# Kernel tuning notes

Measured on AMD Instinct MI355X. Metric: run time of the kernel, lower is better.

Reference implementation:

```python
import jax, jax.numpy as jnp
import numpy as np

B, L, D = 2, 2048, 2048
NUM_HEADS, NUM_KV_HEADS, HEAD_DIM = 8, 4, 256
GROUPS = NUM_HEADS // NUM_KV_HEADS
ROPE_BASE, ROPE_SCALE, ROPE_PROP = 10000.0, 1.0, 1.0
WINDOW = 1024
SOFT_CAP = 50.0
K_MASK = -2.3819763e+38
EPS = 1e-6


def rms_norm(x, scale):
    # RMSNorm(head_dim, with_scale=True, scale_plus_one=False), fp32 internals
    xf = x.astype(jnp.float32)
    var = jnp.mean(jnp.square(xf), axis=-1, keepdims=True)
    return (xf * jax.lax.rsqrt(var + EPS) * scale).astype(x.dtype)


def apply_rope(x, positions):
    # x: [B, L, N, H]; Gemma-style half-split rotation over rope_proportion of H
    H = x.shape[-1]
    rope_dim = int(H * ROPE_PROP)
    half = rope_dim // 2
    freq = ROPE_BASE ** (2.0 * jnp.arange(half, dtype=jnp.float32) / rope_dim)
    t = positions.astype(jnp.float32)[:, :, None] / freq[None, None, :]  # [B,L,half]
    t = t / ROPE_SCALE
    sin = jnp.sin(t)[:, :, None, :]  # [B,L,1,half]
    cos = jnp.cos(t)[:, :, None, :]
    x1 = x[..., :half]
    x2 = x[..., half:rope_dim]
    rotated = jnp.concatenate([x1 * cos - x2 * sin, x2 * cos + x1 * sin], axis=-1)
    if rope_dim < H:
        rotated = jnp.concatenate([rotated, x[..., rope_dim:]], axis=-1)
    return rotated.astype(x.dtype)


def setup_inputs() -> dict:
    key = jax.random.key(0)
    ks = jax.random.split(key, 8)
    x = jax.random.normal(ks[0], (B, L, D), dtype=jnp.float32)
    positions = jnp.broadcast_to(jnp.arange(L, dtype=jnp.int32)[None, :], (B, L))
    attn_mask = jnp.broadcast_to(jnp.tril(jnp.ones((L, L), dtype=bool))[None], (B, L, L))
    s = 0.02
    wq = jax.random.normal(ks[1], (D, NUM_HEADS * HEAD_DIM), dtype=jnp.float32) * s
    wk = jax.random.normal(ks[2], (D, NUM_KV_HEADS * HEAD_DIM), dtype=jnp.float32) * s
    wv = jax.random.normal(ks[3], (D, NUM_KV_HEADS * HEAD_DIM), dtype=jnp.float32) * s
    wo = jax.random.normal(ks[4], (NUM_HEADS * HEAD_DIM, D), dtype=jnp.float32) * s
    q_scale = 1.0 + 0.02 * jax.random.normal(ks[5], (HEAD_DIM,), dtype=jnp.float32)
    k_scale = 1.0 + 0.02 * jax.random.normal(ks[6], (HEAD_DIM,), dtype=jnp.float32)
    return {"x": x, "positions": positions, "attn_mask": attn_mask,
            "wq": wq, "wk": wk, "wv": wv, "wo": wo,
            "q_scale": q_scale, "k_scale": k_scale}


def reference(x, positions, attn_mask, wq, wk, wv, wo, q_scale, k_scale):
    q = (x @ wq).reshape(B, L, NUM_HEADS, HEAD_DIM)
    k = (x @ wk).reshape(B, L, NUM_KV_HEADS, HEAD_DIM)
    v = (x @ wv).reshape(B, L, NUM_KV_HEADS, HEAD_DIM)
    q = rms_norm(q, q_scale)
    k = rms_norm(k, k_scale)
    q = apply_rope(q, positions)
    k = apply_rope(k, positions)
    # query_pre_attn_scalar == 1.0 in source (no-op)
    qg = q.reshape(B, L, NUM_KV_HEADS, GROUPS, HEAD_DIM)
    logits = jnp.einsum('blkgh,bskh->blkgs', qg, k).reshape(B, L, NUM_HEADS, L)
    logits = jnp.tanh(logits / SOFT_CAP) * SOFT_CAP
    # sliding-window mask (LOCAL_SLIDING, no cache -> cache_positions = positions)
    cp = positions[:, None, :]
    pp = positions[:, :, None]
    slide = (cp > pp - WINDOW) & (cp < pp + WINDOW)
    mask = attn_mask & slide  # [B, L, S]
    padded = jnp.where(mask[:, :, None, :], logits, K_MASK)
    probs = jax.nn.softmax(padded, axis=-1).astype(k.dtype)
    pg = probs.reshape(B, L, NUM_KV_HEADS, GROUPS, L)
    out = jnp.einsum('blkgs,bskh->blkgh', pg, v).reshape(B, L, NUM_HEADS * HEAD_DIM)
    return out @ wo
```

## Files before the change

kernel.cpp:

```cpp
#include <hip/hip_runtime.h>
#include <stdint.h>

typedef unsigned short u16;
typedef __bf16 bf16x8 __attribute__((ext_vector_type(8)));
typedef float f32x4 __attribute__((ext_vector_type(4)));

#define SEQ 2048
#define NH 8
#define NKVH 4
#define HD 256
#define WIN 1024
#define NBATCH 2

__device__ __forceinline__ u16 f2bf(float f) {
    union { float f; unsigned u; } v; v.f = f;
    unsigned r = v.u + 0x7FFFu + ((v.u >> 16) & 1u);
    return (u16)(r >> 16);
}
__device__ __forceinline__ float bf2f(u16 h) {
    union { unsigned u; float f; } v; v.u = ((unsigned)h) << 16;
    return v.f;
}
__device__ __forceinline__ bf16x8 ld8(const u16* p) {
    return *reinterpret_cast<const bf16x8*>(p);
}
__device__ __forceinline__ void split2(float f, u16& h, u16& l) {
    h = f2bf(f);
    l = f2bf(f - bf2f(h));
}
__device__ __forceinline__ void gld16(const u16* gp, u16* lp) {
    __builtin_amdgcn_global_load_lds(
        (__attribute__((address_space(1))) unsigned int*)gp,
        (__attribute__((address_space(3))) unsigned int*)lp, 16, 0, 0);
}
#define MFMA16(a, b, c) __builtin_amdgcn_mfma_f32_16x16x32_bf16((a), (b), (c), 0, 0, 0)

__global__ void k_cvt_x(const float* __restrict__ in, u16* __restrict__ hi,
                        u16* __restrict__ lo, int n) {
    int i = (blockIdx.x * blockDim.x + threadIdx.x) * 4;
    if (i >= n) return;
    float4 v = *reinterpret_cast<const float4*>(in + i);
    ushort4 oh, ol;
    split2(v.x, oh.x, ol.x); split2(v.y, oh.y, ol.y);
    split2(v.z, oh.z, ol.z); split2(v.w, oh.w, ol.w);
    *reinterpret_cast<ushort4*>(hi + i) = oh;
    *reinterpret_cast<ushort4*>(lo + i) = ol;
}

__global__ void k_wt(const float* __restrict__ src, u16* __restrict__ dh,
                     u16* __restrict__ dl, int ncols) {
    __shared__ float tile[64][65];
    int c0 = blockIdx.x * 64;
    int k0 = blockIdx.y * 64;
    int tx = threadIdx.x & 63, ty = threadIdx.x >> 6;
    #pragma unroll
    for (int r = 0; r < 16; ++r) {
        int k = k0 + ty * 16 + r;
        tile[ty * 16 + r][tx] = src[(size_t)k * ncols + c0 + tx];
    }
    __syncthreads();
    #pragma unroll
    for (int r = 0; r < 16; ++r) {
        int c = c0 + ty * 16 + r;
        float f = tile[tx][ty * 16 + r];
        u16 h, l; split2(f, h, l);
        dh[(size_t)c * 2048 + k0 + tx] = h;
        dl[(size_t)c * 2048 + k0 + tx] = l;
    }
}

__global__ __launch_bounds__(256, 4) void k_gemm(
        const u16* __restrict__ A0, const u16* __restrict__ B0,
        const u16* __restrict__ A1, const u16* __restrict__ B1,
        const u16* __restrict__ A2, const u16* __restrict__ B2,
        float* __restrict__ C, int M, int N, int K, int nseg, int vcol0) {
    __shared__ __align__(16) u16 sA[128 * 64];
    __shared__ __align__(16) u16 sB[128 * 64];
    const int tm = blockIdx.x * 128;
    const int tn = blockIdx.y * 128;
    const int tid = threadIdx.x;
    const int lane = tid & 63;
    const int wave = tid >> 6;
    const int wr = (wave >> 1) * 64;
    const int wc = (wave & 1) * 64;
    const int l16 = lane & 15;
    const int g = lane >> 4;
    const int srow = tid >> 3;
    const int schunk = tid & 7;
    const int nseg_eff = (tn >= vcol0) ? 1 : nseg;
    f32x4 acc[4][4] = {};

    for (int seg = 0; seg < nseg_eff; ++seg) {
        const u16* A = seg == 0 ? A0 : (seg == 1 ? A1 : A2);
        const u16* B = seg == 0 ? B0 : (seg == 1 ? B1 : B2);
        for (int k0 = 0; k0 < K; k0 += 64) {
            __syncthreads();
            #pragma unroll
            for (int i = 0; i < 4; ++i) {
                int row = i * 32 + srow;
                int cs = ((schunk ^ (row & 7)) << 3);
                gld16(A + (size_t)(tm + row) * K + k0 + cs, &sA[i * 2048 + tid * 8]);
                gld16(B + (size_t)(tn + row) * K + k0 + cs, &sB[i * 2048 + tid * 8]);
            }
            __syncthreads();
            #pragma unroll
            for (int kk = 0; kk < 2; ++kk) {
                const int j = kk * 4 + g;
                bf16x8 af[4], bfv[4];
                #pragma unroll
                for (int m = 0; m < 4; ++m) {
                    int r = wr + m * 16 + l16;
                    af[m] = ld8(&sA[r * 64 + ((j ^ (r & 7)) << 3)]);
                }
                #pragma unroll
                for (int n = 0; n < 4; ++n) {
                    int r = wc + n * 16 + l16;
                    bfv[n] = ld8(&sB[r * 64 + ((j ^ (r & 7)) << 3)]);
                }
                #pragma unroll
                for (int m = 0; m < 4; ++m)
                    #pragma unroll
                    for (int n = 0; n < 4; ++n)
                        acc[m][n] = MFMA16(af[m], bfv[n], acc[m][n]);
            }
        }
    }
    int rbase = tm + wr + g * 4;
    int cbase = tn + wc + l16;
    #pragma unroll
    for (int m = 0; m < 4; ++m)
        #pragma unroll
        for (int n = 0; n < 4; ++n)
            #pragma unroll
            for (int r = 0; r < 4; ++r)
                C[(size_t)(rbase + m * 16 + r) * N + cbase + n * 16] = acc[m][n][r];
}

__global__ void k_normrope(const float* __restrict__ qkv, const int* __restrict__ pos,
                           const float* __restrict__ qscale, const float* __restrict__ kscale,
                           u16* __restrict__ Qh, u16* __restrict__ Ql,
                           u16* __restrict__ Kh, u16* __restrict__ Kl) {
    int wid = blockIdx.x * 4 + (threadIdx.x >> 6);
    int lane = threadIdx.x & 63;
    const int nq = NBATCH * SEQ * NH;
    const int ntot = NBATCH * SEQ * (NH + NKVH);
    if (wid >= ntot) return;
    const float* scale;
    const float* src;
    u16 *dh, *dl;
    int bt, isq;
    if (wid < nq) {
        int h = wid % NH; bt = wid / NH; isq = 1;
        scale = qscale;
        src = qkv + (size_t)bt * 4096 + h * 256;
        int b = bt >> 11, t = bt & 2047;
        size_t off = (((size_t)b * NH + h) * SEQ + t) * 256;
        dh = Qh + off; dl = Ql + off;
    } else {
        int w2 = wid - nq;
        int h = w2 % NKVH; bt = w2 / NKVH; isq = 0;
        scale = kscale;
        src = qkv + (size_t)bt * 4096 + 2048 + h * 256;
        int b = bt >> 11, t = bt & 2047;
        size_t off = (((size_t)b * NKVH + h) * SEQ + t) * 256;
        dh = Kh + off; dl = Kl + off;
    }
    const int t7 = bt & 7;
    float e[4];
    float ssq = 0.f;
    #pragma unroll
    for (int j = 0; j < 4; ++j) { e[j] = src[lane + 64 * j]; ssq += e[j] * e[j]; }
    #pragma unroll
    for (int off = 1; off < 64; off <<= 1) ssq += __shfl_xor(ssq, off);
    float inv = rsqrtf(ssq * (1.0f / 256.0f) + 1e-6f);
    #pragma unroll
    for (int j = 0; j < 4; ++j) e[j] = e[j] * inv * scale[lane + 64 * j];
    float p = (float)pos[bt];
    float fr0 = powf(10000.0f, (2.0f * lane) * (1.0f / 256.0f));
    float fr1 = powf(10000.0f, (2.0f * (lane + 64)) * (1.0f / 256.0f));
    float s0, c0, s1, c1;
    sincosf(p / fr0, &s0, &c0);
    sincosf(p / fr1, &s1, &c1);
    float rv[4];
    rv[0] = e[0] * c0 - e[2] * s0;
    rv[1] = e[1] * c1 - e[3] * s1;
    rv[2] = e[2] * c0 + e[0] * s0;
    rv[3] = e[3] * c1 + e[1] * s1;
    #pragma unroll
    for (int j = 0; j < 4; ++j) {
        int d = lane + 64 * j;
        int dd = isq ? d : ((((d >> 3) ^ t7) << 3) | (d & 7));
        u16 h, l; split2(rv[j], h, l);
        dh[dd] = h; dl[dd] = l;
    }
}

__global__ void k_vtrans(const float* __restrict__ qkv, u16* __restrict__ VT) {
    __shared__ float tile[64][65];
    int bh = blockIdx.z;
    int d0 = blockIdx.y * 64;
    int t0 = blockIdx.x * 64;
    int b = bh >> 2, h = bh & 3;
    int tx = threadIdx.x & 63, ty = threadIdx.x >> 6;
    #pragma unroll
    for (int r = 0; r < 16; ++r) {
        int t = t0 + ty * 16 + r;
        tile[ty * 16 + r][tx] = qkv[(size_t)(b * SEQ + t) * 4096 + 3072 + h * 256 + d0 + tx];
    }
    __syncthreads();
    #pragma unroll
    for (int r = 0; r < 16; ++r) {
        int d = d0 + ty * 16 + r;
        VT[((size_t)bh * 256 + d) * SEQ + t0 + tx] = f2bf(tile[tx][ty * 16 + r]);
    }
}

__global__ __launch_bounds__(256, 2) void k_attn(const u16* __restrict__ Qh, const u16* __restrict__ Ql,
                                                 const u16* __restrict__ Kh, const u16* __restrict__ Kl,
                                                 const u16* __restrict__ VT,
                                                 u16* __restrict__ Out) {
    __shared__ __align__(16) u16 sKh[32 * 256];
    __shared__ __align__(16) u16 sKl[32 * 256];
    __shared__ __align__(16) u16 sV[256 * 32];
    __shared__ __align__(16) u16 pls[4][16][40];

    const int id = blockIdx.x;
    const int xcd = id & 7;
    const int j = id >> 3;
    const int b  = xcd >> 2;
    const int hk = xcd & 3;
    const int hq = hk * 2 + (j & 1);
    const int qt = 31 - (j >> 1);
    const int tid = threadIdx.x;
    const int lane = tid & 63;
    const int wave = tid >> 6;
    const int q0b = qt * 64;
    const int q0 = q0b + wave * 16;
    const int l16 = lane & 15;
    const int g = lane >> 4;

    bf16x8 qfh[8], qfl[8];
    {
        size_t qoff = (((size_t)b * NH + hq) * SEQ + q0 + l16) * 256 + g * 8;
        #pragma unroll
        for (int kk = 0; kk < 8; ++kk) {
            qfh[kk] = ld8(Qh + qoff + kk * 32);
            qfl[kk] = ld8(Ql + qoff + kk * 32);
        }
    }

    float ssum[4] = {0.f, 0.f, 0.f, 0.f};
    f32x4 o[16] = {};

    const u16* kgh = Kh + (((size_t)b * NKVH + hk) * SEQ) * 256;
    const u16* kgl = Kl + (((size_t)b * NKVH + hk) * SEQ) * 256;
    const u16* vg  = VT + ((size_t)(b * NKVH + hk) * 256) * SEQ;

    int s_lo = q0b - (WIN - 1); if (s_lo < 0) s_lo = 0; s_lo &= ~31;
    const int s_hi = q0b + 63;
    const int ntiles = (s_hi - s_lo) / 32 + 1;

    for (int t = 0; t < ntiles; ++t) {
        const int s0 = s_lo + t * 32;
        __syncthreads();
        {
            const u16* srch = kgh + (size_t)s0 * 256 + tid * 8;
            const u16* srcl = kgl + (size_t)s0 * 256 + tid * 8;
            #pragma unroll
            for (int i = 0; i < 4; ++i) {
                gld16(srch + i * 2048, &sKh[i * 2048 + tid * 8]);
                gld16(srcl + i * 2048, &sKl[i * 2048 + tid * 8]);
            }
            const u16* srcv = vg + (size_t)(tid >> 2) * SEQ + s0 + (tid & 3) * 8;
            #pragma unroll
            for (int i = 0; i < 4; ++i)
                gld16(srcv + (size_t)i * 64 * SEQ, &sV[i * 2048 + tid * 8]);
        }
        __syncthreads();

        if (s0 <= q0 + 15 && s0 + 31 >= q0 - (WIN - 1)) {
            f32x4 c[2] = {};
            __builtin_amdgcn_s_setprio(1);
            #pragma unroll
            for (int kk = 0; kk < 8; ++kk) {
                #pragma unroll
                for (int cc = 0; cc < 2; ++cc) {
                    int row = cc * 16 + l16;
                    int slot = ((kk * 4 + g) ^ (row & 7)) << 3;
                    bf16x8 kh = ld8(&sKh[row * 256 + slot]);
                    bf16x8 kl = ld8(&sKl[row * 256 + slot]);
                    c[cc] = MFMA16(qfh[kk], kh, c[cc]);
                    c[cc] = MFMA16(qfl[kk], kh, c[cc]);
                    c[cc] = MFMA16(qfh[kk], kl, c[cc]);
                }
            }
            __builtin_amdgcn_s_setprio(0);

            const bool full = (s0 + 31 <= q0) && (s0 >= q0 + 15 - (WIN - 1));
            #pragma unroll
            for (int r = 0; r < 4; ++r) {
                int qp = q0 + g * 4 + r;
                int row = g * 4 + r;
                #pragma unroll
                for (int cc = 0; cc < 2; ++cc) {
                    float ev = __expf(c[cc][r] * 0.04f);
                    float v = 50.f - 100.f * __builtin_amdgcn_rcpf(ev + 1.f);
                    if (!full) {
                        int sp = s0 + cc * 16 + l16;
                        bool valid = (sp <= qp) && (sp > qp - WIN);
                        v = valid ? v : -1e30f;
                    }
                    float p = __expf(v - 20.f);
                    u16 pb = f2bf(p);
                    pls[wave][row][cc * 16 + l16] = pb;
                    ssum[r] += bf2f(pb);
                }
            }
            bf16x8 pa = ld8(&pls[wave][l16][g * 8]);
            __builtin_amdgcn_s_setprio(1);
            #pragma unroll
            for (int jb = 0; jb < 16; ++jb)
                o[jb] = MFMA16(pa, ld8(&sV[(jb * 16 + l16) * 32 + g * 8]), o[jb]);
            __builtin_amdgcn_s_setprio(0);
        }
    }

    #pragma unroll
    for (int off = 1; off < 16; off <<= 1)
        #pragma unroll
        for (int r = 0; r < 4; ++r) ssum[r] += __shfl_xor(ssum[r], off);
    #pragma unroll
    for (int r = 0; r < 4; ++r) {
        float inv = 1.0f / ssum[r];
        int trow = q0 + g * 4 + r;
        size_t base = ((size_t)(b * SEQ + trow) * NH + hq) * 256 + l16;
        #pragma unroll
        for (int jb = 0; jb < 16; ++jb)
            Out[base + jb * 16] = f2bf(o[jb][r] * inv);
    }
}

extern "C" void kernel_launch(void* const* d_in, const int* in_sizes, int n_in,
                              void* d_out, int out_size, void* d_ws, size_t ws_size,
                              hipStream_t stream) {
    (void)in_sizes; (void)n_in; (void)out_size; (void)ws_size;
    const float* x  = (const float*)d_in[0];
    const int* pos  = (const int*)d_in[1];
    const float* wq = (const float*)d_in[3];
    const float* wk = (const float*)d_in[4];
    const float* wv = (const float*)d_in[5];
    const float* wo = (const float*)d_in[6];
    const float* qs = (const float*)d_in[7];
    const float* ks = (const float*)d_in[8];

    const size_t MX = (size_t)4096 * 2048;
    const size_t MW = (size_t)2048 * 2048;

    u16* xh  = (u16*)d_ws;
    u16* xl  = xh + MX;
    u16* wth = xl + MX;
    u16* wtl = wth + MX;
    u16* woth = wtl + MX;
    u16* wotl = woth + MW;
    float* qkv = (float*)(wotl + MW);

    u16* qbh = xh;
    u16* qbl = qbh + MX;
    u16* kbh = qbl + MX;
    u16* kbl = kbh + MX / 2;
    u16* vt  = kbl + MX / 2;
    u16* ao  = (u16*)qkv;

    k_cvt_x<<<8192, 256, 0, stream>>>(x, xh, xl, 4096 * 2048);
    k_wt<<<dim3(32, 32), 256, 0, stream>>>(wq, wth, wtl, 2048);
    k_wt<<<dim3(16, 32), 256, 0, stream>>>(wk, wth + MW, wtl + MW, 1024);
    k_wt<<<dim3(16, 32), 256, 0, stream>>>(wv, wth + MW + MW / 2, wtl + MW + MW / 2, 1024);
    k_wt<<<dim3(32, 32), 256, 0, stream>>>(wo, woth, wotl, 2048);
    k_gemm<<<dim3(32, 32), 256, 0, stream>>>(xh, wth, xl, wth, xh, wtl, qkv,
                                             4096, 4096, 2048, 3, 3072);
    k_normrope<<<12288, 256, 0, stream>>>(qkv, pos, qs, ks, qbh, qbl, kbh, kbl);
    k_vtrans<<<dim3(32, 4, 8), 256, 0, stream>>>(qkv, vt);
    k_attn<<<512, 256, 0, stream>>>(qbh, qbl, kbh, kbl, vt, ao);
    k_gemm<<<dim3(32, 16), 256, 0, stream>>>(ao, woth, ao, woth, ao, wotl, (float*)d_out,
                                             4096, 2048, 2048, 1, 2048);
}
```

Before: 394.8 us.

## Add 256x256-tile double-buffered GEMM for the QKV projection

Adds a new GEMM kernel with 256x256 output tiles, 512 threads and a double-buffered LDS pipeline that prefetches the next K slice while the MFMAs run on the current one. It replaces the 128-tile GEMM for the split-bf16 QKV projection. Larger tiles raise operand reuse and cut global traffic, and the prefetch hides load latency. In exchange it uses 128KB of LDS per block and more accumulator registers, and launches only 256 blocks, which lowers occupancy and may leave CUs underfilled.

```diff
diff --git a/kernel.cpp b/kernel.cpp
--- a/kernel.cpp
+++ b/kernel.cpp
@@ -129,6 +129,96 @@
     int cbase = tn + wc + l16;
     #pragma unroll
     for (int m = 0; m < 4; ++m)
+        #pragma unroll
+        for (int n = 0; n < 4; ++n)
+            #pragma unroll
+            for (int r = 0; r < 4; ++r)
+                C[(size_t)(rbase + m * 16 + r) * N + cbase + n * 16] = acc[m][n][r];
+}
+
+__global__ __launch_bounds__(512, 2) void k_gemm256(
+        const u16* __restrict__ A0, const u16* __restrict__ B0,
+        const u16* __restrict__ A1, const u16* __restrict__ B1,
+        const u16* __restrict__ A2, const u16* __restrict__ B2,
+        float* __restrict__ C, int N, int K, int nseg, int vcol0) {
+    __shared__ __align__(16) u16 sA[2][256 * 64];
+    __shared__ __align__(16) u16 sB[2][256 * 64];
+    const int tm = blockIdx.x * 256;
+    const int tn = blockIdx.y * 256;
+    const int tid = threadIdx.x;
+    const int lane = tid & 63;
+    const int wave = tid >> 6;
+    const int wr = (wave >> 2) * 128;
+    const int wc = (wave & 3) * 64;
+    const int l16 = lane & 15;
+    const int g = lane >> 4;
+    const int nsteps = ((tn >= vcol0) ? 1 : nseg) * (K >> 6);
+    const int spk = K >> 6;
+    f32x4 acc[8][4] = {};
+
+    {
+        const u16* A = A0; const u16* B = B0;
+        #pragma unroll
+        for (int i = 0; i < 4; ++i) {
+            int s = i * 512 + tid;
+            int row = s >> 3, ch = s & 7;
+            int cs = (ch ^ (row & 7)) << 3;
+            gld16(A + (size_t)(tm + row) * K + cs, &sA[0][s * 8]);
+            gld16(B + (size_t)(tn + row) * K + cs, &sB[0][s * 8]);
+        }
+    }
+    asm volatile("s_waitcnt vmcnt(0)" ::: "memory");
+    __builtin_amdgcn_s_barrier();
+
+    int p = 0;
+    for (int t = 0; t < nsteps; ++t) {
+        if (t + 1 < nsteps) {
+            int t1 = t + 1;
+            int seg = t1 / spk;
+            int k0 = (t1 - seg * spk) * 64;
+            const u16* A = seg == 0 ? A0 : (seg == 1 ? A1 : A2);
+            const u16* B = seg == 0 ? B0 : (seg == 1 ? B1 : B2);
+            #pragma unroll
+            for (int i = 0; i < 4; ++i) {
+                int s = i * 512 + tid;
+                int row = s >> 3, ch = s & 7;
+                int cs = (ch ^ (row & 7)) << 3;
+                gld16(A + (size_t)(tm + row) * K + k0 + cs, &sA[p ^ 1][s * 8]);
+                gld16(B + (size_t)(tn + row) * K + k0 + cs, &sB[p ^ 1][s * 8]);
+            }
+        }
+        __builtin_amdgcn_s_setprio(1);
+        bf16x8 bfv[4][2];
+        #pragma unroll
+        for (int n = 0; n < 4; ++n)
+            #pragma unroll
+            for (int kk = 0; kk < 2; ++kk) {
+                int r = wc + n * 16 + l16;
+                int j = kk * 4 + g;
+                bfv[n][kk] = ld8(&sB[p][r * 64 + ((j ^ (r & 7)) << 3)]);
+            }
+        #pragma unroll
+        for (int m = 0; m < 8; ++m) {
+            int r = wr + m * 16 + l16;
+            bf16x8 af0 = ld8(&sA[p][r * 64 + (((0 * 4 + g) ^ (r & 7)) << 3)]);
+            bf16x8 af1 = ld8(&sA[p][r * 64 + (((1 * 4 + g) ^ (r & 7)) << 3)]);
+            #pragma unroll
+            for (int n = 0; n < 4; ++n) {
+                acc[m][n] = MFMA16(af0, bfv[n][0], acc[m][n]);
+                acc[m][n] = MFMA16(af1, bfv[n][1], acc[m][n]);
+            }
+        }
+        __builtin_amdgcn_s_setprio(0);
+        asm volatile("s_waitcnt vmcnt(0) lgkmcnt(0)" ::: "memory");
+        __builtin_amdgcn_sched_barrier(0);
+        __builtin_amdgcn_s_barrier();
+        p ^= 1;
+    }
+
+    int rbase = tm + wr + g * 4;
+    int cbase = tn + wc + l16;
+    #pragma unroll
+    for (int m = 0; m < 8; ++m)
         #pragma unroll
         for (int n = 0; n < 4; ++n)
             #pragma unroll
@@ -376,8 +466,8 @@
     k_wt<<<dim3(16, 32), 256, 0, stream>>>(wk, wth + MW, wtl + MW, 1024);
     k_wt<<<dim3(16, 32), 256, 0, stream>>>(wv, wth + MW + MW / 2, wtl + MW + MW / 2, 1024);
     k_wt<<<dim3(32, 32), 256, 0, stream>>>(wo, woth, wotl, 2048);
-    k_gemm<<<dim3(32, 32), 256, 0, stream>>>(xh, wth, xl, wth, xh, wtl, qkv,
-                                             4096, 4096, 2048, 3, 3072);
+    k_gemm256<<<dim3(16, 16), 512, 0, stream>>>(xh, wth, xl, wth, xh, wtl, qkv,
+                                                4096, 2048, 3, 3072);
     k_normrope<<<12288, 256, 0, stream>>>(qkv, pos, qs, ks, qbh, qbl, kbh, kbl);
     k_vtrans<<<dim3(32, 4, 8), 256, 0, stream>>>(qkv, vt);
     k_attn<<<512, 256, 0, stream>>>(qbh, qbl, kbh, kbl, vt, ao);
```

After: 381.9 us. -3.3%, faster.
